# Kernel optimization log

Measured on AMD Instinct MI355X. Metric: run time of the kernel, lower is better.

The kernel has to match this reference:

```python
import jax, jax.numpy as jnp
import numpy as np

NUM_MASHUP = 50000
NUM_API = 50000
NUM_DOMAIN = 500
MC = 768   # mashup_embed_channels
AC = 768   # api_embed_channels
DC = 768   # domain_embed_channels
FEAT = 128 # feature_dim
BETA = 0.5
NLAYERS = 3
E = 1600000  # bipartite invocations (one direction)
BATCH = 1024


def setup_inputs() -> dict:
    key = jax.random.key(0)
    ks = jax.random.split(key, 16)
    s = 0.02
    return {
        "x": jax.random.normal(ks[0], (BATCH, MC), dtype=jnp.float32),
        "mashup_embed": jax.random.normal(ks[1], (NUM_MASHUP, MC), dtype=jnp.float32),
        "domain_embed": jax.random.normal(ks[2], (NUM_DOMAIN, DC), dtype=jnp.float32),
        "api_embed": jax.random.normal(ks[3], (NUM_API, AC), dtype=jnp.float32),
        "W_sde": jax.random.normal(ks[4], (MC, FEAT), dtype=jnp.float32) * s,
        "b_sde": jnp.zeros((FEAT,), jnp.float32),
        "W_val": jax.random.normal(ks[5], (DC, FEAT), dtype=jnp.float32) * s,
        "b_val": jnp.zeros((FEAT,), jnp.float32),
        "W_key": jax.random.normal(ks[6], (DC, FEAT), dtype=jnp.float32) * s,
        "b_key": jnp.zeros((FEAT,), jnp.float32),
        "W_sie": jax.random.normal(ks[7], (AC, FEAT), dtype=jnp.float32) * s,
        "b_sie": jnp.zeros((FEAT,), jnp.float32),
        "edge_src": jax.random.randint(ks[8], (E,), 0, NUM_MASHUP, dtype=jnp.int32),
        "edge_dst": jax.random.randint(ks[9], (E,), 0, NUM_API, dtype=jnp.int32),
    }


def _sig_lin(h, W, b):
    # nn.Linear + Sigmoid
    return jax.nn.sigmoid(h @ W + b)


def _lightgcn(emb, row, col, num_nodes, num_layers):
    # PyG LightGCN.get_embedding: mean of layer-0..L embeddings with
    # symmetric gcn_norm propagation over the bipartite graph.
    ones = jnp.ones(row.shape, emb.dtype)
    deg = jax.ops.segment_sum(ones, row, num_segments=num_nodes)
    dinv = jnp.where(deg > 0, jax.lax.rsqrt(deg), 0.0)
    norm = dinv[row] * dinv[col]  # [2E]
    alpha = 1.0 / (num_layers + 1)
    x_l = emb
    out = emb * alpha
    for _ in range(num_layers):
        # message x[row]*norm scattered to col (graph is symmetric)
        x_l = jax.ops.segment_sum(x_l[row] * norm[:, None], col, num_segments=num_nodes)
        out = out + x_l * alpha
    return out


def reference(x, mashup_embed, domain_embed, api_embed,
              W_sde, b_sde, W_val, b_val, W_key, b_key, W_sie, b_sie,
              edge_src, edge_dst):
    batch = x.shape[0]
    # --- attention pooling over domain embeddings (SDE branch) ---
    v_mi = _sig_lin(x, W_sde, b_sde)                 # [B, F]
    v_value = _sig_lin(domain_embed, W_val, b_val)   # [D, F]
    v_key = _sig_lin(domain_embed, W_key, b_key)     # [D, F]
    al = v_mi @ v_key.T                              # [B, D]
    alpha = al / jnp.sum(al, axis=1, keepdims=True)  # normalized (no softmax)
    s_m = alpha @ v_value                            # [B, F]
    z_m = (1.0 - BETA) * s_m + BETA * v_mi           # [B, F]
    # --- LightGCN propagation over mashup-api bipartite graph ---
    v_m = _sig_lin(mashup_embed, W_sde, b_sde)       # [Nm, F]
    v_s = _sig_lin(api_embed, W_sie, b_sie)          # [Na, F]
    emb = jnp.concatenate([v_m, v_s], axis=0)        # [N, F]
    num_nodes = NUM_MASHUP + NUM_API
    src = edge_src.astype(jnp.int32)
    dst = edge_dst.astype(jnp.int32) + NUM_MASHUP
    row = jnp.concatenate([src, dst])                # [2E] symmetric edges
    col = jnp.concatenate([dst, src])
    out = _lightgcn(emb, row, col, num_nodes, NLAYERS)
    O = out[NUM_MASHUP:]                             # [Na, F]
    # --- dot-product scoring ---
    pred = z_m @ O.T                                 # [B, Na]
    return pred
```

## Files before the change

kernel.cpp:

```cpp
#include <hip/hip_runtime.h>
#include <hip/hip_bf16.h>
#include <cstddef>
#include <cstdint>

#define NM 50000
#define NA 50000
#define ND 500
#define FEAT 128
#define KDIM 768
#define BATCH 1024
#define NEDGE 1600000
#define MD 128

#define NBIN 196
#define CAP 10240
#define F1B 400
#define F1E (NEDGE / F1B)

#define PBLK 391

typedef __bf16 bf16_t;
typedef bf16_t bf16x8 __attribute__((ext_vector_type(8)));
typedef bf16_t bf16x4 __attribute__((ext_vector_type(4)));
typedef float f32x4 __attribute__((ext_vector_type(4)));
typedef float f32x2 __attribute__((ext_vector_type(2)));
typedef unsigned short u16;
typedef unsigned char u8;

__device__ __forceinline__ float sigf(float x) { return 1.0f / (1.0f + __expf(-x)); }

__device__ __forceinline__ float4 dec4fp8(uint32_t w) {
  f32x2 lo = __builtin_amdgcn_cvt_pk_f32_fp8(w, false);
  f32x2 hi = __builtin_amdgcn_cvt_pk_f32_fp8(w, true);
  return make_float4(lo[0], lo[1], hi[0], hi[1]);
}
__device__ __forceinline__ u8 enc1fp8(float a) {
  return (u8)(__builtin_amdgcn_cvt_pk_fp8_f32(a, a, 0, false) & 0xff);
}

__global__ __launch_bounds__(256) void fill_bin(
    const int* __restrict__ src, const int* __restrict__ dst,
    int* __restrict__ bcur, uint32_t* __restrict__ rec )
{
  __shared__ uint32_t edg[F1E];
  __shared__ int hist[2 * NBIN];
  __shared__ int base[2 * NBIN];
  const int tid = threadIdx.x;
  for (int i = tid; i < 2 * NBIN; i += 256) hist[i] = 0;
  __syncthreads();
  const int e0 = blockIdx.x * F1E;
  for (int i = tid; i < F1E; i += 256) {
    int s = __builtin_nontemporal_load(&src[e0 + i]);
    int d = __builtin_nontemporal_load(&dst[e0 + i]);
    edg[i] = ((uint32_t)s << 16) | (uint32_t)d;
    atomicAdd(&hist[s >> 8], 1);
    atomicAdd(&hist[NBIN + (d >> 8)], 1);
  }
  __syncthreads();
  for (int i = tid; i < 2 * NBIN; i += 256) {
    int c = hist[i];
    base[i] = c ? atomicAdd(&bcur[i], c) : 0;
    hist[i] = 0;
  }
  __syncthreads();
  for (int i = tid; i < F1E; i += 256) {
    uint32_t e = edg[i];
    int s = (int)(e >> 16), d = (int)(e & 0xffffu);
    int bm = s >> 8, ba = NBIN + (d >> 8);
    int rm = base[bm] + atomicAdd(&hist[bm], 1);
    int ra = base[ba] + atomicAdd(&hist[ba], 1);
    if (rm < CAP) rec[(size_t)bm * CAP + rm] = e;
    if (ra < CAP) rec[(size_t)ba * CAP + ra] = ((uint32_t)d << 16) | (uint32_t)s;
  }
}

__global__ __launch_bounds__(256) void fill_ell2(
    const uint32_t* __restrict__ rec, const int* __restrict__ bcur,
    u16* __restrict__ adjm, u16* __restrict__ adja,
    int* __restrict__ cnt_m, int* __restrict__ cnt_a)
{
  __shared__ int cnt256[256];
  const int g = blockIdx.x;
  const int side = g >= NBIN;
  const int bin = side ? g - NBIN : g;
  u16* adj = side ? adja : adjm;
  int* cnt = side ? cnt_a : cnt_m;
  cnt256[threadIdx.x] = 0;
  __syncthreads();
  int n = bcur[g]; if (n > CAP) n = CAP;
  const uint32_t* rb = rec + (size_t)g * CAP;
  for (int i = threadIdx.x; i < n; i += 256) {
    uint32_t r = rb[i];
    int node = (int)(r >> 16);
    int rk = atomicAdd(&cnt256[node & 255], 1);
    if (rk < MD) adj[(size_t)node * MD + rk] = (u16)(r & 0xffffu);
  }
  __syncthreads();
  int node = bin * 256 + threadIdx.x;
  if (node < NM) cnt[node] = cnt256[threadIdx.x];
}

__global__ __launch_bounds__(256) void util_kernel(
    const float* __restrict__ W0, const float* __restrict__ W1,
    const float* __restrict__ W2, const float* __restrict__ W3,
    bf16_t* __restrict__ T0, bf16_t* __restrict__ T1,
    bf16_t* __restrict__ T2, bf16_t* __restrict__ T3,
    const int* __restrict__ cnt_m, const int* __restrict__ cnt_a,
    float* __restrict__ dm, float* __restrict__ da)
{
  const int b = blockIdx.x;
  if (b < 512) {
    const float* W = (b < 128) ? W0 : (b < 256) ? W1 : (b < 384) ? W2 : W3;
    bf16_t* T      = (b < 128) ? T0 : (b < 256) ? T1 : (b < 384) ? T2 : T3;
    int c = b & 127;
    for (int k = threadIdx.x; k < KDIM; k += 256)
      T[(size_t)c * KDIM + k] = (bf16_t)W[(size_t)k * FEAT + c];
  } else {
    int i = (b - 512) * 256 + threadIdx.x;
    if (i < NM) { int c = cnt_m[i]; dm[i] = c > 0 ? rsqrtf((float)c) : 0.f; }
    if (i < NA) { int c = cnt_a[i]; da[i] = c > 0 ? rsqrtf((float)c) : 0.f; }
  }
}

template<int OM>
__device__ __forceinline__ void proj_body(
    const float* __restrict__ A, const bf16_t* __restrict__ Wt,
    const float* __restrict__ bias, void* __restrict__ Cout, int M, int rowBase,
    const float* __restrict__ rowscale, bf16_t* __restrict__ C2)
{
  __shared__ bf16x8 sm[1024];
  const int tid = threadIdx.x;
  const int lane = tid & 63;
  const int wid = tid >> 6;

  f32x4 acc[4][4];
  #pragma unroll
  for (int m = 0; m < 4; ++m)
    #pragma unroll
    for (int n = 0; n < 4; ++n)
      acc[m][n] = (f32x4){0.f, 0.f, 0.f, 0.f};

  const int rl0 = ((tid >> 6) << 4) + (tid & 15);
  const int k8 = (tid >> 4) & 3;

  for (int k0 = 0; k0 < KDIM; k0 += 32) {
    #pragma unroll
    for (int i = 0; i < 2; ++i) {
      int rloc = rl0 + 64 * i;
      int rg = rowBase + rloc;
      if (rg > M - 1) rg = M - 1;
      const float* ap = A + (size_t)rg * KDIM + k0 + k8 * 8;
      float4 v0 = *(const float4*)ap;
      float4 v1 = *(const float4*)(ap + 4);
      bf16x8 w;
      w[0] = (bf16_t)v0.x; w[1] = (bf16_t)v0.y; w[2] = (bf16_t)v0.z; w[3] = (bf16_t)v0.w;
      w[4] = (bf16_t)v1.x; w[5] = (bf16_t)v1.y; w[6] = (bf16_t)v1.z; w[7] = (bf16_t)v1.w;
      sm[tid + i * 256] = w;
      sm[512 + tid + i * 256] = *(const bf16x8*)(Wt + (size_t)rloc * KDIM + k0 + k8 * 8);
    }
    __syncthreads();
    bf16x8 a[4], b[4];
    const int fm = (wid >> 1) * 4, fn = (wid & 1) * 4;
    #pragma unroll
    for (int m = 0; m < 4; ++m) a[m] = sm[(fm + m) * 64 + lane];
    #pragma unroll
    for (int n = 0; n < 4; ++n) b[n] = sm[512 + (fn + n) * 64 + lane];
    #pragma unroll
    for (int m = 0; m < 4; ++m)
      #pragma unroll
      for (int n = 0; n < 4; ++n)
        acc[m][n] = __builtin_amdgcn_mfma_f32_16x16x32_bf16(a[m], b[n], acc[m][n], 0, 0, 0);
    __syncthreads();
  }

  const int wRow = (wid >> 1) * 64, wCol = (wid & 1) * 64;
  const int r0 = (lane >> 4) * 4, cc = lane & 15;
  #pragma unroll
  for (int n = 0; n < 4; ++n) {
    int col = wCol + n * 16 + cc;
    float bb = bias[col];
    #pragma unroll
    for (int m = 0; m < 4; ++m) {
      #pragma unroll
      for (int r = 0; r < 4; ++r) {
        int row = rowBase + wRow + m * 16 + r0 + r;
        if (row < M) {
          float v = sigf(acc[m][n][r] + bb);
          float sc = rowscale ? rowscale[row] : 1.0f;
          if constexpr (OM == 2)
            ((u8*)Cout)[(size_t)row * FEAT + col] = enc1fp8(v * sc);
          else
            ((float*)Cout)[(size_t)row * FEAT + col] = v * sc;
          if (C2) C2[(size_t)row * FEAT + col] = (bf16_t)(0.25f * v);
        }
      }
    }
  }
}

__global__ __launch_bounds__(256) void proj_all(
    const float* __restrict__ mashup, const float* __restrict__ api,
    const float* __restrict__ x, const float* __restrict__ domain,
    const bf16_t* __restrict__ wt0, const bf16_t* __restrict__ wt1,
    const bf16_t* __restrict__ wt2, const bf16_t* __restrict__ wt3,
    const float* __restrict__ bsde, const float* __restrict__ bkey,
    const float* __restrict__ bval, const float* __restrict__ bsie,
    u8* __restrict__ M0y8, u8* __restrict__ y0a8,
    float* __restrict__ vmi, float* __restrict__ vkey, float* __restrict__ vval,
    const float* __restrict__ dm, const float* __restrict__ da,
    bf16_t* __restrict__ outA)
{
  const int b = blockIdx.x;
  if (b < PBLK)
    proj_body<2>(mashup, wt0, bsde, M0y8, NM, b * 128, dm, nullptr);
  else if (b < 2 * PBLK)
    proj_body<2>(api, wt3, bsie, y0a8, NA, (b - PBLK) * 128, da, outA);
  else if (b < 2 * PBLK + 8)
    proj_body<0>(x, wt0, bsde, vmi, BATCH, (b - 2 * PBLK) * 128, nullptr, nullptr);
  else if (b < 2 * PBLK + 12)
    proj_body<0>(domain, wt1, bkey, vkey, ND, (b - 2 * PBLK - 8) * 128, nullptr, nullptr);
  else
    proj_body<0>(domain, wt2, bval, vval, ND, (b - 2 * PBLK - 12) * 128, nullptr, nullptr);
}

__global__ __launch_bounds__(256) void attn_kernel(
    const float* __restrict__ vmi, const float* __restrict__ vkey,
    const float* __restrict__ vval, bf16_t* __restrict__ zm)
{
  const int i = blockIdx.x;
  const int tid = threadIdx.x;
  __shared__ float vs[FEAT];
  __shared__ float al[ND];
  __shared__ float red[4];
  __shared__ float ps[256];
  __shared__ float totS;
  if (tid < FEAT) vs[tid] = vmi[(size_t)i * FEAT + tid];
  __syncthreads();
  float part = 0.f;
  for (int j = tid; j < ND; j += 256) {
    const float* kr = vkey + (size_t)j * FEAT;
    float dot = 0.f;
    #pragma unroll 8
    for (int k = 0; k < FEAT; k += 4) {
      float4 kv = *(const float4*)(kr + k);
      dot += vs[k] * kv.x + vs[k + 1] * kv.y + vs[k + 2] * kv.z + vs[k + 3] * kv.w;
    }
    al[j] = dot;
    part += dot;
  }
  #pragma unroll
  for (int o = 32; o > 0; o >>= 1) part += __shfl_down(part, o, 64);
  if ((tid & 63) == 0) red[tid >> 6] = part;
  __syncthreads();
  if (tid == 0) totS = red[0] + red[1] + red[2] + red[3];
  const int f = tid & 127, h = tid >> 7;
  float s = 0.f;
  const float* vv = vval + (size_t)h * 250 * FEAT + f;
  #pragma unroll 5
  for (int j = 0; j < 250; ++j) s += al[h * 250 + j] * vv[(size_t)j * FEAT];
  ps[tid] = s;
  __syncthreads();
  if (tid < FEAT) {
    float z = 0.5f * ((ps[tid] + ps[128 + tid]) / totS + vs[tid]);
    zm[(size_t)i * FEAT + tid] = (bf16_t)z;
  }
}

__device__ __forceinline__ float4 gatherF8(const uint32_t* __restrict__ base32,
                                           const u16* __restrict__ row,
                                           int n, int half)
{
  float4 acc = make_float4(0.f, 0.f, 0.f, 0.f);
  int j = half;
  while (j + 14 < n) {
    int u[8];
    #pragma unroll
    for (int q = 0; q < 8; ++q) u[q] = row[j + 2 * q];
    uint32_t w[8];
    #pragma unroll
    for (int q = 0; q < 8; ++q) w[q] = base32[(size_t)u[q] * 32];
    #pragma unroll
    for (int q = 0; q < 8; ++q) {
      float4 v = dec4fp8(w[q]);
      acc.x += v.x; acc.y += v.y; acc.z += v.z; acc.w += v.w;
    }
    j += 16;
  }
  while (j < n) {
    float4 v = dec4fp8(base32[(size_t)row[j] * 32]);
    acc.x += v.x; acc.y += v.y; acc.z += v.z; acc.w += v.w;
    j += 2;
  }
  return acc;
}

#define REDUCE_HALVES(acc)                    \
  acc.x += __shfl_xor(acc.x, 32);             \
  acc.y += __shfl_xor(acc.y, 32);             \
  acc.z += __shfl_xor(acc.z, 32);             \
  acc.w += __shfl_xor(acc.w, 32);

__global__ __launch_bounds__(256) void prop_p1(
    const uint32_t* __restrict__ M0y8, const uint32_t* __restrict__ y0a8,
    uint32_t* __restrict__ y01a8,
    const u16* __restrict__ adja, const int* __restrict__ cnt_a,
    const float* __restrict__ da)
{
  const int a = blockIdx.x * 4 + (threadIdx.x >> 6);
  const int lane = threadIdx.x & 63;
  const int half = lane >> 5, sl = lane & 31;
  int n = cnt_a[a]; if (n > MD) n = MD;
  float4 acc = gatherF8(M0y8 + sl, adja + (size_t)a * MD, n, half);
  REDUCE_HALVES(acc)
  if (half == 0) {
    const float d = da[a];
    const float s2 = d * d;
    float4 b = dec4fp8(y0a8[(size_t)a * 32 + sl]);
    uint32_t o = __builtin_amdgcn_cvt_pk_fp8_f32(b.x + s2 * acc.x, b.y + s2 * acc.y, 0, false);
    o = __builtin_amdgcn_cvt_pk_fp8_f32(b.z + s2 * acc.z, b.w + s2 * acc.w, o, true);
    y01a8[(size_t)a * 32 + sl] = o;
  }
}

__global__ __launch_bounds__(256) void prop_p2(
    const uint32_t* __restrict__ y01a8, const uint32_t* __restrict__ M0y8,
    uint32_t* __restrict__ Sy8,
    const u16* __restrict__ adjm, const int* __restrict__ cnt_m,
    const float* __restrict__ dm)
{
  const int m = blockIdx.x * 4 + (threadIdx.x >> 6);
  const int lane = threadIdx.x & 63;
  const int half = lane >> 5, sl = lane & 31;
  int n = cnt_m[m]; if (n > MD) n = MD;
  float4 acc = gatherF8(y01a8 + sl, adjm + (size_t)m * MD, n, half);
  REDUCE_HALVES(acc)
  if (half == 0) {
    const float d = dm[m];
    const float s2 = d * d;
    float4 b = dec4fp8(M0y8[(size_t)m * 32 + sl]);
    uint32_t o = __builtin_amdgcn_cvt_pk_fp8_f32(b.x + s2 * acc.x, b.y + s2 * acc.y, 0, false);
    o = __builtin_amdgcn_cvt_pk_fp8_f32(b.z + s2 * acc.z, b.w + s2 * acc.w, o, true);
    Sy8[(size_t)m * 32 + sl] = o;
  }
}

__global__ __launch_bounds__(256) void prop_p3(
    const uint32_t* __restrict__ Sy8, const bf16_t* __restrict__ outA,
    bf16_t* __restrict__ Obf,
    const u16* __restrict__ adja, const int* __restrict__ cnt_a,
    const float* __restrict__ da)
{
  const int a = blockIdx.x * 4 + (threadIdx.x >> 6);
  const int lane = threadIdx.x & 63;
  const int half = lane >> 5, sl = lane & 31;
  int n = cnt_a[a]; if (n > MD) n = MD;
  float4 acc = gatherF8(Sy8 + sl, adja + (size_t)a * MD, n, half);
  REDUCE_HALVES(acc)
  if (half == 0) {
    const float q = 0.25f * da[a];
    bf16x4 pv = *(const bf16x4*)(outA + (size_t)a * FEAT + 4 * sl);
    bf16x4 o;
    o[0] = (bf16_t)((float)pv[0] + q * acc.x);
    o[1] = (bf16_t)((float)pv[1] + q * acc.y);
    o[2] = (bf16_t)((float)pv[2] + q * acc.z);
    o[3] = (bf16_t)((float)pv[3] + q * acc.w);
    *(bf16x4*)(Obf + (size_t)a * FEAT + 4 * sl) = o;
  }
}

__global__ __launch_bounds__(256) void pred_mfma(
    const bf16_t* __restrict__ Z, const bf16_t* __restrict__ O,
    float* __restrict__ out)
{
  const int lane = threadIdx.x & 63;
  const int wid = threadIdx.x >> 6;
  const int nBase = blockIdx.x * 256 + wid * 64;
  const int cc = lane & 15;
  const int kOff = (lane >> 4) * 8;

  bf16x8 b[4][4];
  #pragma unroll
  for (int n = 0; n < 4; ++n) {
    int c = nBase + n * 16 + cc;
    if (c > NA - 1) c = NA - 1;
    #pragma unroll
    for (int kk = 0; kk < 4; ++kk)
      b[n][kk] = *(const bf16x8*)(O + (size_t)c * FEAT + kk * 32 + kOff);
  }

  const int r0 = (lane >> 4) * 4;
  #pragma unroll
  for (int it = 0; it < 4; ++it) {
    const int iBase = blockIdx.y * 256 + it * 64;
    f32x4 acc[4][4];
    #pragma unroll
    for (int m = 0; m < 4; ++m)
      #pragma unroll
      for (int n = 0; n < 4; ++n)
        acc[m][n] = (f32x4){0.f, 0.f, 0.f, 0.f};

    #pragma unroll
    for (int kk = 0; kk < 4; ++kk) {
      bf16x8 a[4];
      #pragma unroll
      for (int m = 0; m < 4; ++m)
        a[m] = *(const bf16x8*)(Z + (size_t)(iBase + cc + m * 16) * FEAT + kk * 32 + kOff);
      #pragma unroll
      for (int m = 0; m < 4; ++m)
        #pragma unroll
        for (int n = 0; n < 4; ++n)
          acc[m][n] = __builtin_amdgcn_mfma_f32_16x16x32_bf16(a[m], b[n][kk], acc[m][n], 0, 0, 0);
    }

    #pragma unroll
    for (int n = 0; n < 4; ++n) {
      int col = nBase + n * 16 + cc;
      if (col < NA) {
        #pragma unroll
        for (int m = 0; m < 4; ++m) {
          #pragma unroll
          for (int r = 0; r < 4; ++r) {
            int row = iBase + m * 16 + r0 + r;
            __builtin_nontemporal_store(acc[m][n][r], &out[(size_t)row * NA + col]);
          }
        }
      }
    }
  }
}

static inline char* alignup(char* p, size_t a) {
  return (char*)(((uintptr_t)p + a - 1) & ~(uintptr_t)(a - 1));
}

extern "C" void kernel_launch(void* const* d_in, const int* in_sizes, int n_in,
                              void* d_out, int out_size, void* d_ws, size_t ws_size,
                              hipStream_t stream) {
  const float* x      = (const float*)d_in[0];
  const float* mashup = (const float*)d_in[1];
  const float* domain = (const float*)d_in[2];
  const float* api    = (const float*)d_in[3];
  const float* Wsde   = (const float*)d_in[4];
  const float* bsde   = (const float*)d_in[5];
  const float* Wval   = (const float*)d_in[6];
  const float* bval   = (const float*)d_in[7];
  const float* Wkey   = (const float*)d_in[8];
  const float* bkey   = (const float*)d_in[9];
  const float* Wsie   = (const float*)d_in[10];
  const float* bsie   = (const float*)d_in[11];
  const int* esrc     = (const int*)d_in[12];
  const int* edst     = (const int*)d_in[13];
  float* out = (float*)d_out;

  char* p = (char*)d_ws;
  u8*     M0y8  = (u8*)p; p += (size_t)NM * FEAT;
  u8*     y0a8  = (u8*)p; p += (size_t)NA * FEAT;
  u8*     y01a8 = (u8*)p; p += (size_t)NA * FEAT;
  u8*     Sy8   = (u8*)p; p += (size_t)NM * FEAT;
  bf16_t* outA  = (bf16_t*)p; p += (size_t)NA * FEAT * 2;
  bf16_t* Obf   = (bf16_t*)p; p += (size_t)NA * FEAT * 2;
  u16*    adjm  = (u16*)p;    p += (size_t)NM * MD * 2;
  u16*    adja  = (u16*)p;    p += (size_t)NA * MD * 2;
  float*  vmi   = (float*)p;  p += (size_t)BATCH * FEAT * 4;
  float*  vkey  = (float*)p;  p += (size_t)ND * FEAT * 4;
  float*  vval  = (float*)p;  p += (size_t)ND * FEAT * 4;
  bf16_t* zm    = (bf16_t*)p; p += (size_t)BATCH * FEAT * 2;
  int* cnt_m = (int*)p; p += (size_t)NM * 4;
  int* cnt_a = (int*)p; p += (size_t)NA * 4;
  float* dm  = (float*)p; p += (size_t)NM * 4;
  float* da  = (float*)p; p += (size_t)NA * 4;
  int* bcur  = (int*)p; p += 512 * 4;
  p = alignup(p, 16);
  bf16_t* wt0 = (bf16_t*)p; p += (size_t)FEAT * KDIM * 2;
  bf16_t* wt1 = (bf16_t*)p; p += (size_t)FEAT * KDIM * 2;
  bf16_t* wt2 = (bf16_t*)p; p += (size_t)FEAT * KDIM * 2;
  bf16_t* wt3 = (bf16_t*)p; p += (size_t)FEAT * KDIM * 2;
  uint32_t* rec = (uint32_t*)M0y8;

  hipMemsetAsync(bcur, 0, 512 * sizeof(int), stream);

  fill_bin<<<F1B, 256, 0, stream>>>(esrc, edst, bcur, rec);
  fill_ell2<<<2 * NBIN, 256, 0, stream>>>(rec, bcur, adjm, adja, cnt_m, cnt_a);
  util_kernel<<<512 + (NM + 255) / 256, 256, 0, stream>>>(
      Wsde, Wkey, Wval, Wsie, wt0, wt1, wt2, wt3, cnt_m, cnt_a, dm, da);

  proj_all<<<2 * PBLK + 16, 256, 0, stream>>>(
      mashup, api, x, domain, wt0, wt1, wt2, wt3,
      bsde, bkey, bval, bsie, M0y8, y0a8, vmi, vkey, vval, dm, da, outA);

  attn_kernel<<<BATCH, 256, 0, stream>>>(vmi, vkey, vval, zm);

  prop_p1<<<NA / 4, 256, 0, stream>>>((const uint32_t*)M0y8, (const uint32_t*)y0a8,
                                      (uint32_t*)y01a8, adja, cnt_a, da);
  prop_p2<<<NM / 4, 256, 0, stream>>>((const uint32_t*)y01a8, (const uint32_t*)M0y8,
                                      (uint32_t*)Sy8, adjm, cnt_m, dm);
  prop_p3<<<NA / 4, 256, 0, stream>>>((const uint32_t*)Sy8, outA, Obf,
                                      adja, cnt_a, da);

  pred_mfma<<<dim3((NA + 255) / 256, BATCH / 256), 256, 0, stream>>>(zm, Obf, out);
}
```

Before: 429.9 us.

## Halve projection tile rows and prefetch next K-slice into registers

```diff
diff --git a/kernel.cpp b/kernel.cpp
--- a/kernel.cpp
+++ b/kernel.cpp
@@ -17,7 +17,7 @@
 #define F1B 400
 #define F1E (NEDGE / F1B)
 
-#define PBLK 391
+#define PB64 782
 
 typedef __bf16 bf16_t;
 typedef bf16_t bf16x8 __attribute__((ext_vector_type(8)));
@@ -128,59 +128,68 @@
     const float* __restrict__ bias, void* __restrict__ Cout, int M, int rowBase,
     const float* __restrict__ rowscale, bf16_t* __restrict__ C2)
 {
-  __shared__ bf16x8 sm[1024];
+  __shared__ bf16x8 sm[768];
   const int tid = threadIdx.x;
   const int lane = tid & 63;
   const int wid = tid >> 6;
 
-  f32x4 acc[4][4];
+  f32x4 acc[2][4];
   #pragma unroll
-  for (int m = 0; m < 4; ++m)
+  for (int m = 0; m < 2; ++m)
     #pragma unroll
     for (int n = 0; n < 4; ++n)
       acc[m][n] = (f32x4){0.f, 0.f, 0.f, 0.f};
 
-  const int rl0 = ((tid >> 6) << 4) + (tid & 15);
+  const int arow = ((tid >> 6) << 4) + (tid & 15);
   const int k8 = (tid >> 4) & 3;
-
-  for (int k0 = 0; k0 < KDIM; k0 += 32) {
-    #pragma unroll
-    for (int i = 0; i < 2; ++i) {
-      int rloc = rl0 + 64 * i;
-      int rg = rowBase + rloc;
-      if (rg > M - 1) rg = M - 1;
-      const float* ap = A + (size_t)rg * KDIM + k0 + k8 * 8;
-      float4 v0 = *(const float4*)ap;
-      float4 v1 = *(const float4*)(ap + 4);
-      bf16x8 w;
-      w[0] = (bf16_t)v0.x; w[1] = (bf16_t)v0.y; w[2] = (bf16_t)v0.z; w[3] = (bf16_t)v0.w;
-      w[4] = (bf16_t)v1.x; w[5] = (bf16_t)v1.y; w[6] = (bf16_t)v1.z; w[7] = (bf16_t)v1.w;
-      sm[tid + i * 256] = w;
-      sm[512 + tid + i * 256] = *(const bf16x8*)(Wt + (size_t)rloc * KDIM + k0 + k8 * 8);
+  int arg = rowBase + arow; if (arg > M - 1) arg = M - 1;
+  const float*  aptr  = A  + (size_t)arg * KDIM + k8 * 8;
+  const bf16_t* bptr0 = Wt + (size_t)arow * KDIM + k8 * 8;
+  const bf16_t* bptr1 = Wt + (size_t)(arow + 64) * KDIM + k8 * 8;
+
+  float4 pa0 = *(const float4*)aptr;
+  float4 pa1 = *(const float4*)(aptr + 4);
+  bf16x8 pb0 = *(const bf16x8*)bptr0;
+  bf16x8 pb1 = *(const bf16x8*)bptr1;
+
+  const int fm0 = (wid >> 1) * 2, fn0 = (wid & 1) * 4;
+
+  for (int kt = 0; kt < KDIM / 32; ++kt) {
+    bf16x8 w;
+    w[0] = (bf16_t)pa0.x; w[1] = (bf16_t)pa0.y; w[2] = (bf16_t)pa0.z; w[3] = (bf16_t)pa0.w;
+    w[4] = (bf16_t)pa1.x; w[5] = (bf16_t)pa1.y; w[6] = (bf16_t)pa1.z; w[7] = (bf16_t)pa1.w;
+    sm[tid] = w;
+    sm[256 + tid] = pb0;
+    sm[512 + tid] = pb1;
+    __syncthreads();
+    if (kt + 1 < KDIM / 32) {
+      const int ko = (kt + 1) * 32;
+      pa0 = *(const float4*)(aptr + ko);
+      pa1 = *(const float4*)(aptr + ko + 4);
+      pb0 = *(const bf16x8*)(bptr0 + ko);
+      pb1 = *(const bf16x8*)(bptr1 + ko);
     }
-    __syncthreads();
-    bf16x8 a[4], b[4];
-    const int fm = (wid >> 1) * 4, fn = (wid & 1) * 4;
-    #pragma unroll
-    for (int m = 0; m < 4; ++m) a[m] = sm[(fm + m) * 64 + lane];
-    #pragma unroll
-    for (int n = 0; n < 4; ++n) b[n] = sm[512 + (fn + n) * 64 + lane];
-    #pragma unroll
-    for (int m = 0; m < 4; ++m)
+    bf16x8 a[2], b[4];
+    #pragma unroll
+    for (int m = 0; m < 2; ++m) a[m] = sm[(fm0 + m) * 64 + lane];
+    #pragma unroll
+    for (int n = 0; n < 4; ++n) b[n] = sm[256 + (fn0 + n) * 64 + lane];
+    #pragma unroll
+    for (int m = 0; m < 2; ++m)
       #pragma unroll
       for (int n = 0; n < 4; ++n)
         acc[m][n] = __builtin_amdgcn_mfma_f32_16x16x32_bf16(a[m], b[n], acc[m][n], 0, 0, 0);
     __syncthreads();
   }
 
-  const int wRow = (wid >> 1) * 64, wCol = (wid & 1) * 64;
+  const int wRow = (wid >> 1) * 32, wCol = (wid & 1) * 64;
   const int r0 = (lane >> 4) * 4, cc = lane & 15;
   #pragma unroll
   for (int n = 0; n < 4; ++n) {
     int col = wCol + n * 16 + cc;
     float bb = bias[col];
     #pragma unroll
-    for (int m = 0; m < 4; ++m) {
+    for (int m = 0; m < 2; ++m) {
       #pragma unroll
       for (int r = 0; r < 4; ++r) {
         int row = rowBase + wRow + m * 16 + r0 + r;
@@ -211,16 +220,16 @@
     bf16_t* __restrict__ outA)
 {
   const int b = blockIdx.x;
-  if (b < PBLK)
-    proj_body<2>(mashup, wt0, bsde, M0y8, NM, b * 128, dm, nullptr);
-  else if (b < 2 * PBLK)
-    proj_body<2>(api, wt3, bsie, y0a8, NA, (b - PBLK) * 128, da, outA);
-  else if (b < 2 * PBLK + 8)
-    proj_body<0>(x, wt0, bsde, vmi, BATCH, (b - 2 * PBLK) * 128, nullptr, nullptr);
-  else if (b < 2 * PBLK + 12)
-    proj_body<0>(domain, wt1, bkey, vkey, ND, (b - 2 * PBLK - 8) * 128, nullptr, nullptr);
+  if (b < PB64)
+    proj_body<2>(mashup, wt0, bsde, M0y8, NM, b * 64, dm, nullptr);
+  else if (b < 2 * PB64)
+    proj_body<2>(api, wt3, bsie, y0a8, NA, (b - PB64) * 64, da, outA);
+  else if (b < 2 * PB64 + 16)
+    proj_body<0>(x, wt0, bsde, vmi, BATCH, (b - 2 * PB64) * 64, nullptr, nullptr);
+  else if (b < 2 * PB64 + 24)
+    proj_body<0>(domain, wt1, bkey, vkey, ND, (b - 2 * PB64 - 16) * 64, nullptr, nullptr);
   else
-    proj_body<0>(domain, wt2, bval, vval, ND, (b - 2 * PBLK - 12) * 128, nullptr, nullptr);
+    proj_body<0>(domain, wt2, bval, vval, ND, (b - 2 * PB64 - 24) * 64, nullptr, nullptr);
 }
 
 __global__ __launch_bounds__(256) void attn_kernel(
@@ -484,7 +493,7 @@
   util_kernel<<<512 + (NM + 255) / 256, 256, 0, stream>>>(
       Wsde, Wkey, Wval, Wsie, wt0, wt1, wt2, wt3, cnt_m, cnt_a, dm, da);
 
-  proj_all<<<2 * PBLK + 16, 256, 0, stream>>>(
+  proj_all<<<2 * PB64 + 32, 256, 0, stream>>>(
       mashup, api, x, domain, wt0, wt1, wt2, wt3,
       bsde, bkey, bval, bsie, M0y8, y0a8, vmi, vkey, vval, dm, da, outA);
 
```

Measured after the change: 421.3 us. 1.02x faster.
